# Kernel optimization log

Hardware: AMD Instinct MI355X
Metric: run time of the kernel (lower is better)

Reference implementation:

```python
import jax, jax.numpy as jnp
import numpy as np

B, T = 32768, 32
OBJ_V, PRED_V = 179, 46
E_OBJ, E_PRED, H = 5, 5, 32
IN_DIM = E_OBJ + E_PRED + 2 + 4  # 16, matches LSTMCell input size


def setup_inputs() -> dict:
    key = jax.random.key(0)
    ks = jax.random.split(key, 12)
    s = 0.1
    return {
        "input_objects": jax.random.randint(ks[0], (B, T), 0, OBJ_V),
        "input_boxes": jax.random.uniform(ks[1], (B, T, 4), dtype=jnp.float32),
        "predicates": jax.random.randint(ks[2], (B, T), 0, PRED_V),
        "subject_indicators": jax.random.randint(ks[3], (B, T), 0, 2),
        "target_object": jax.random.randint(ks[4], (B,), 0, OBJ_V),
        "obj_emb": jax.random.normal(ks[5], (OBJ_V, E_OBJ), dtype=jnp.float32) * s,
        "pred_emb": jax.random.normal(ks[6], (PRED_V, E_PRED), dtype=jnp.float32) * s,
        "W_ih": jax.random.normal(ks[7], (4 * H, IN_DIM), dtype=jnp.float32) * s,
        "W_hh": jax.random.normal(ks[8], (4 * H, H), dtype=jnp.float32) * s,
        "b_ih": jnp.zeros((4 * H,), dtype=jnp.float32),
        "b_hh": jnp.zeros((4 * H,), dtype=jnp.float32),
        "fc2_W": jax.random.normal(ks[9], (4, H), dtype=jnp.float32) * s,
        "fc2_b": jnp.zeros((4,), dtype=jnp.float32),
    }


def _forward(input_objects, input_boxes, predicates, subject_indicators,
             obj_emb, pred_emb, W_ih, W_hh, b_ih, b_hh, fc2_W, fc2_b):
    # concatenate_features, vectorized over all timesteps at once: [B,T,16]
    feats = jnp.concatenate([
        obj_emb[input_objects],                                   # [B,T,5]
        pred_emb[predicates],                                     # [B,T,5]
        jax.nn.one_hot(subject_indicators, 2, dtype=jnp.float32), # [B,T,2]
        input_boxes,                                              # [B,T,4]
    ], axis=-1)
    xs = jnp.transpose(feats, (1, 0, 2))  # [T,B,16] for scan over time

    def step(carry, x):
        h, c = carry
        gates = x @ W_ih.T + b_ih + h @ W_hh.T + b_hh  # [B,4H]
        i, f, g, o = jnp.split(gates, 4, axis=-1)      # torch gate order i,f,g,o
        i = jax.nn.sigmoid(i)
        f = jax.nn.sigmoid(f)
        g = jnp.tanh(g)
        o = jax.nn.sigmoid(o)
        c = f * c + i * g
        h = o * jnp.tanh(c)
        return (h, c), None

    h0 = jnp.zeros((input_objects.shape[0], H), dtype=jnp.float32)
    (h, _), _ = jax.lax.scan(step, (h0, h0), xs)
    out = h @ fc2_W.T + fc2_b          # output_fc2 on last hidden state
    return jnp.clip(out, 0.0, 1.0)     # torch.clamp(min=0, max=1)


def reference(input_objects, input_boxes, predicates, subject_indicators, target_object,
              obj_emb, pred_emb, W_ih, W_hh, b_ih, b_hh, fc2_W, fc2_b):
    # target_object is accepted by the torch forward but unused in its body
    return _forward(input_objects, input_boxes, predicates, subject_indicators,
                    obj_emb, pred_emb, W_ih, W_hh, b_ih, b_hh, fc2_W, fc2_b)
```

## Files before the change

### kernel.cpp

```cpp
#include <hip/hip_runtime.h>

#define XSTRIDE 1072
#define ZOFF    (16 * XSTRIDE)
#define LDS_BYTES (ZOFF + 32)

typedef _Float16 f16x8 __attribute__((ext_vector_type(8)));
typedef __fp16   fp16x2 __attribute__((ext_vector_type(2)));
typedef float    f32x4 __attribute__((ext_vector_type(4)));
typedef float    f32x2 __attribute__((ext_vector_type(2)));

#define LOG2E     1.44269504088896f
#define TWO_LOG2E 2.88539008177793f

__global__ __launch_bounds__(64, 2)
void lstm_fused(const int* __restrict__ objs,
                const float* __restrict__ boxes,
                const int* __restrict__ preds,
                const int* __restrict__ subj,
                const float* __restrict__ obj_emb,
                const float* __restrict__ pred_emb,
                const float* __restrict__ W_ih,
                const float* __restrict__ W_hh,
                const float* __restrict__ b_ih,
                const float* __restrict__ b_hh,
                const float* __restrict__ fc2_W,
                const float* __restrict__ fc2_b,
                float* __restrict__ out)
{
    extern __shared__ char smem[];
    const int lane = threadIdx.x;
    const int quad = lane >> 4;
    const int cidx = lane & 15;

    if (lane < 8) ((int*)(smem + ZOFF))[lane] = 0;

    {
        const int b = lane >> 2;
        const int j = lane & 3;
        const long gb = (long)blockIdx.x * 16 + b;
        const int* orow = objs + gb * 32;
        const int* prow = preds + gb * 32;
        const int* srow = subj + gb * 32;
        const float* brow = boxes + gb * 128;
        char* xrow = smem + b * XSTRIDE;
        #pragma unroll
        for (int tt = 0; tt < 8; ++tt) {
            int t = j + tt * 4;
            int o = orow[t], p = prow[t], sv = srow[t];
            const float* eo = obj_emb + o * 5;
            const float* ep = pred_emb + p * 5;
            float4 bx = *(const float4*)(brow + t * 4);
            f16x8 lo, hi;
            lo[0]=(_Float16)eo[0]; lo[1]=(_Float16)eo[1]; lo[2]=(_Float16)eo[2];
            lo[3]=(_Float16)eo[3]; lo[4]=(_Float16)eo[4];
            lo[5]=(_Float16)ep[0]; lo[6]=(_Float16)ep[1]; lo[7]=(_Float16)ep[2];
            hi[0]=(_Float16)ep[3]; hi[1]=(_Float16)ep[4];
            hi[2]=(_Float16)(sv==0 ? 1.0f : 0.0f);
            hi[3]=(_Float16)(sv==1 ? 1.0f : 0.0f);
            hi[4]=(_Float16)bx.x; hi[5]=(_Float16)bx.y;
            hi[6]=(_Float16)bx.z; hi[7]=(_Float16)bx.w;
            *(f16x8*)(xrow + t * 32)      = lo;
            *(f16x8*)(xrow + t * 32 + 16) = hi;
        }
    }

    f16x8 WH[8], WX[8];
    f32x4 bias[8];
    #pragma unroll
    for (int a = 0; a < 8; ++a) {
        const int gate = a >> 1;
        const float scale = (gate == 2) ? TWO_LOG2E : -LOG2E;
        const int n = gate * 32 + 8 * (cidx >> 2) + 4 * (a & 1) + (cidx & 3);
        const float* wr = W_hh + n * 32 + quad * 8;
        float4 w0 = *(const float4*)(wr);
        float4 w1 = *(const float4*)(wr + 4);
        f16x8 h8;
        h8[0]=(_Float16)(w0.x*scale); h8[1]=(_Float16)(w0.y*scale);
        h8[2]=(_Float16)(w0.z*scale); h8[3]=(_Float16)(w0.w*scale);
        h8[4]=(_Float16)(w1.x*scale); h8[5]=(_Float16)(w1.y*scale);
        h8[6]=(_Float16)(w1.z*scale); h8[7]=(_Float16)(w1.w*scale);
        WH[a] = h8;
        f16x8 x8;
        if (quad < 2) {
            const float* xr = W_ih + n * 16 + quad * 8;
            float4 u0 = *(const float4*)(xr);
            float4 u1 = *(const float4*)(xr + 4);
            x8[0]=(_Float16)(u0.x*scale); x8[1]=(_Float16)(u0.y*scale);
            x8[2]=(_Float16)(u0.z*scale); x8[3]=(_Float16)(u0.w*scale);
            x8[4]=(_Float16)(u1.x*scale); x8[5]=(_Float16)(u1.y*scale);
            x8[6]=(_Float16)(u1.z*scale); x8[7]=(_Float16)(u1.w*scale);
        } else {
            #pragma unroll
            for (int jj = 0; jj < 8; ++jj) x8[jj] = (_Float16)0.0f;
        }
        WX[a] = x8;
        const int nb = gate * 32 + 8 * quad + 4 * (a & 1);
        float4 bi = *(const float4*)(b_ih + nb);
        float4 bh = *(const float4*)(b_hh + nb);
        f32x4 bb = {(bi.x+bh.x)*scale, (bi.y+bh.y)*scale,
                    (bi.z+bh.z)*scale, (bi.w+bh.w)*scale};
        bias[a] = bb;
    }

    __syncthreads();

    const bool qlow = (quad < 2);
    int xaddr = qlow ? (cidx * XSTRIDE + quad * 16) : ZOFF;
    const int xinc = qlow ? 32 : 0;

    f16x8 xfrag = *(const f16x8*)(smem + xaddr); xaddr += xinc;
    f32x4 accp[8];
    #pragma unroll
    for (int a = 0; a < 8; ++a)
        accp[a] = __builtin_amdgcn_mfma_f32_16x16x32_f16(WX[a], xfrag, bias[a], 0, 0, 0);

    union { int i[4]; f16x8 v; } hf;
    hf.i[0]=0; hf.i[1]=0; hf.i[2]=0; hf.i[3]=0;
    const f32x2 zz = {0.0f, 0.0f};
    f32x2 cst[4] = {zz, zz, zz, zz};
    f32x2 hv[4];
    const f32x2 one = {1.0f, 1.0f};

    #pragma unroll 1
    for (int t = 0; t < 32; ++t) {
        f32x4 acc[8];
        #pragma unroll
        for (int a = 0; a < 8; ++a)
            acc[a] = __builtin_amdgcn_mfma_f32_16x16x32_f16(WH[a], hf.v, accp[a], 0, 0, 0);

        f16x8 xn = *(const f16x8*)(smem + xaddr); xaddr += xinc;

        #pragma unroll
        for (int cc = 0; cc < 4; ++cc) {
            const int sel = cc >> 1;
            const int r0  = (cc & 1) << 1;
            f32x2 zi = {acc[0+sel][r0], acc[0+sel][r0+1]};
            f32x2 zf = {acc[2+sel][r0], acc[2+sel][r0+1]};
            f32x2 zg = {acc[4+sel][r0], acc[4+sel][r0+1]};
            f32x2 zo = {acc[6+sel][r0], acc[6+sel][r0+1]};
            f32x2 Ei = {__builtin_amdgcn_exp2f(zi.x), __builtin_amdgcn_exp2f(zi.y)};
            f32x2 Ef = {__builtin_amdgcn_exp2f(zf.x), __builtin_amdgcn_exp2f(zf.y)};
            f32x2 Eg = {__builtin_amdgcn_exp2f(zg.x), __builtin_amdgcn_exp2f(zg.y)};
            f32x2 Eo = {__builtin_amdgcn_exp2f(zo.x), __builtin_amdgcn_exp2f(zo.y)};
            f32x2 t1  = Ei + one;
            f32x2 dig = t1 * Eg + t1;
            f32x2 tf  = Ef + one;
            f32x2 nn  = (Eg - one) * tf + cst[cc] * dig;
            f32x2 den = tf * dig;
            f32x2 rde = {__builtin_amdgcn_rcpf(den.x), __builtin_amdgcn_rcpf(den.y)};
            f32x2 c   = nn * rde;
            cst[cc] = c;
            f32x2 cl  = c * TWO_LOG2E;
            f32x2 Ec  = {__builtin_amdgcn_exp2f(cl.x), __builtin_amdgcn_exp2f(cl.y)};
            f32x2 to  = Eo + one;
            f32x2 dh  = to * Ec + to;
            f32x2 rdh = {__builtin_amdgcn_rcpf(dh.x), __builtin_amdgcn_rcpf(dh.y)};
            hv[cc] = (Ec - one) * rdh;
            union { fp16x2 h; int i; } pk;
            pk.h = __builtin_amdgcn_cvt_pkrtz(hv[cc].x, hv[cc].y);
            hf.i[cc] = pk.i;
        }

        #pragma unroll
        for (int a = 0; a < 8; ++a)
            accp[a] = __builtin_amdgcn_mfma_f32_16x16x32_f16(WX[a], xn, bias[a], 0, 0, 0);
    }

    __syncthreads();
    {
        char* s0 = smem + cidx * 144 + quad * 32;
        float4 lo4 = {hv[0].x, hv[0].y, hv[1].x, hv[1].y};
        float4 hi4 = {hv[2].x, hv[2].y, hv[3].x, hv[3].y};
        *(float4*)s0        = lo4;
        *(float4*)(s0 + 16) = hi4;
    }
    __syncthreads();
    {
        const int b = lane >> 2, j = lane & 3;
        const float* hrow = (const float*)(smem + b * 144);
        const float* fw = fc2_W + j * 32;
        float s = fc2_b[j];
        #pragma unroll
        for (int k = 0; k < 8; ++k) {
            float4 hvv = *(const float4*)(hrow + k * 4);
            float4 wv4 = *(const float4*)(fw + k * 4);
            s += wv4.x*hvv.x + wv4.y*hvv.y + wv4.z*hvv.z + wv4.w*hvv.w;
        }
        s = fminf(fmaxf(s, 0.0f), 1.0f);
        out[(long)blockIdx.x * 64 + lane] = s;
    }
}

extern "C" void kernel_launch(void* const* d_in, const int* in_sizes, int n_in,
                              void* d_out, int out_size, void* d_ws, size_t ws_size,
                              hipStream_t stream)
{
    lstm_fused<<<2048, 64, LDS_BYTES, stream>>>(
        (const int*)d_in[0], (const float*)d_in[1], (const int*)d_in[2],
        (const int*)d_in[3],
        (const float*)d_in[5], (const float*)d_in[6],
        (const float*)d_in[7], (const float*)d_in[8],
        (const float*)d_in[9], (const float*)d_in[10],
        (const float*)d_in[11], (const float*)d_in[12],
        (float*)d_out);
}
```

Baseline: 129.5 us.

## Switch LSTM recurrence to 32x32x16 MFMA with 32 batch rows per wave

Each wave now processes 32 batch rows instead of 16, using 32x32x16 f16 MFMA. The recurrent matmul splits into two chained MFMAs per gate over hidden halves, and the input projection needs no zero-padded fragment. Gate rows are permuted so each lane's accumulator rows line up with the next step's B-operand layout. The final FC is done in registers with a cross-half shuffle instead of an LDS round trip. The grid is halved and launch bounds drop to one wave per EU, which cuts parallelism across CUs and lengthens the serial chain per wave.

Result: slower. 135.7 us (+4.8%).

```diff
diff --git a/kernel.cpp b/kernel.cpp
--- a/kernel.cpp
+++ b/kernel.cpp
@@ -1,18 +1,27 @@
 #include <hip/hip_runtime.h>
 
-#define XSTRIDE 1072
-#define ZOFF    (16 * XSTRIDE)
-#define LDS_BYTES (ZOFF + 32)
+#define XSTRIDE 1040
+#define LDS_BYTES (32 * XSTRIDE)
 
 typedef _Float16 f16x8 __attribute__((ext_vector_type(8)));
 typedef __fp16   fp16x2 __attribute__((ext_vector_type(2)));
-typedef float    f32x4 __attribute__((ext_vector_type(4)));
+typedef float    f32x16 __attribute__((ext_vector_type(16)));
 typedef float    f32x2 __attribute__((ext_vector_type(2)));
 
 #define LOG2E     1.44269504088896f
 #define TWO_LOG2E 2.88539008177793f
 
-__global__ __launch_bounds__(64, 2)
+static __device__ __forceinline__ f16x8 cvt8(float4 a, float4 b, float s)
+{
+    f16x8 r;
+    r[0]=(_Float16)(a.x*s); r[1]=(_Float16)(a.y*s);
+    r[2]=(_Float16)(a.z*s); r[3]=(_Float16)(a.w*s);
+    r[4]=(_Float16)(b.x*s); r[5]=(_Float16)(b.y*s);
+    r[6]=(_Float16)(b.z*s); r[7]=(_Float16)(b.w*s);
+    return r;
+}
+
+__global__ __launch_bounds__(64, 1)
 void lstm_fused(const int* __restrict__ objs,
                 const float* __restrict__ boxes,
                 const int* __restrict__ preds,
@@ -29,115 +38,100 @@
 {
     extern __shared__ char smem[];
     const int lane = threadIdx.x;
-    const int quad = lane >> 4;
-    const int cidx = lane & 15;
-
-    if (lane < 8) ((int*)(smem + ZOFF))[lane] = 0;
+    const int hi   = lane >> 5;
+    const int col  = lane & 31;
 
     {
-        const int b = lane >> 2;
-        const int j = lane & 3;
-        const long gb = (long)blockIdx.x * 16 + b;
+        const int b = lane >> 1;
+        const int j = lane & 1;
+        const long gb = (long)blockIdx.x * 32 + b;
         const int* orow = objs + gb * 32;
         const int* prow = preds + gb * 32;
         const int* srow = subj + gb * 32;
         const float* brow = boxes + gb * 128;
         char* xrow = smem + b * XSTRIDE;
         #pragma unroll
-        for (int tt = 0; tt < 8; ++tt) {
-            int t = j + tt * 4;
+        for (int tt = 0; tt < 16; ++tt) {
+            int t = j + tt * 2;
             int o = orow[t], p = prow[t], sv = srow[t];
             const float* eo = obj_emb + o * 5;
             const float* ep = pred_emb + p * 5;
             float4 bx = *(const float4*)(brow + t * 4);
-            f16x8 lo, hi;
-            lo[0]=(_Float16)eo[0]; lo[1]=(_Float16)eo[1]; lo[2]=(_Float16)eo[2];
-            lo[3]=(_Float16)eo[3]; lo[4]=(_Float16)eo[4];
-            lo[5]=(_Float16)ep[0]; lo[6]=(_Float16)ep[1]; lo[7]=(_Float16)ep[2];
-            hi[0]=(_Float16)ep[3]; hi[1]=(_Float16)ep[4];
-            hi[2]=(_Float16)(sv==0 ? 1.0f : 0.0f);
-            hi[3]=(_Float16)(sv==1 ? 1.0f : 0.0f);
-            hi[4]=(_Float16)bx.x; hi[5]=(_Float16)bx.y;
-            hi[6]=(_Float16)bx.z; hi[7]=(_Float16)bx.w;
-            *(f16x8*)(xrow + t * 32)      = lo;
-            *(f16x8*)(xrow + t * 32 + 16) = hi;
-        }
-    }
-
-    f16x8 WH[8], WX[8];
-    f32x4 bias[8];
-    #pragma unroll
-    for (int a = 0; a < 8; ++a) {
-        const int gate = a >> 1;
-        const float scale = (gate == 2) ? TWO_LOG2E : -LOG2E;
-        const int n = gate * 32 + 8 * (cidx >> 2) + 4 * (a & 1) + (cidx & 3);
-        const float* wr = W_hh + n * 32 + quad * 8;
-        float4 w0 = *(const float4*)(wr);
-        float4 w1 = *(const float4*)(wr + 4);
-        f16x8 h8;
-        h8[0]=(_Float16)(w0.x*scale); h8[1]=(_Float16)(w0.y*scale);
-        h8[2]=(_Float16)(w0.z*scale); h8[3]=(_Float16)(w0.w*scale);
-        h8[4]=(_Float16)(w1.x*scale); h8[5]=(_Float16)(w1.y*scale);
-        h8[6]=(_Float16)(w1.z*scale); h8[7]=(_Float16)(w1.w*scale);
-        WH[a] = h8;
-        f16x8 x8;
-        if (quad < 2) {
-            const float* xr = W_ih + n * 16 + quad * 8;
-            float4 u0 = *(const float4*)(xr);
-            float4 u1 = *(const float4*)(xr + 4);
-            x8[0]=(_Float16)(u0.x*scale); x8[1]=(_Float16)(u0.y*scale);
-            x8[2]=(_Float16)(u0.z*scale); x8[3]=(_Float16)(u0.w*scale);
-            x8[4]=(_Float16)(u1.x*scale); x8[5]=(_Float16)(u1.y*scale);
-            x8[6]=(_Float16)(u1.z*scale); x8[7]=(_Float16)(u1.w*scale);
-        } else {
-            #pragma unroll
-            for (int jj = 0; jj < 8; ++jj) x8[jj] = (_Float16)0.0f;
-        }
-        WX[a] = x8;
-        const int nb = gate * 32 + 8 * quad + 4 * (a & 1);
-        float4 bi = *(const float4*)(b_ih + nb);
-        float4 bh = *(const float4*)(b_hh + nb);
-        f32x4 bb = {(bi.x+bh.x)*scale, (bi.y+bh.y)*scale,
-                    (bi.z+bh.z)*scale, (bi.w+bh.w)*scale};
-        bias[a] = bb;
+            f16x8 lo8, hi8;
+            lo8[0]=(_Float16)eo[0]; lo8[1]=(_Float16)eo[1]; lo8[2]=(_Float16)eo[2];
+            lo8[3]=(_Float16)eo[3]; lo8[4]=(_Float16)eo[4];
+            lo8[5]=(_Float16)ep[0]; lo8[6]=(_Float16)ep[1]; lo8[7]=(_Float16)ep[2];
+            hi8[0]=(_Float16)ep[3]; hi8[1]=(_Float16)ep[4];
+            hi8[2]=(_Float16)(sv==0 ? 1.0f : 0.0f);
+            hi8[3]=(_Float16)(sv==1 ? 1.0f : 0.0f);
+            hi8[4]=(_Float16)bx.x; hi8[5]=(_Float16)bx.y;
+            hi8[6]=(_Float16)bx.z; hi8[7]=(_Float16)bx.w;
+            *(f16x8*)(xrow + t * 32)      = lo8;
+            *(f16x8*)(xrow + t * 32 + 16) = hi8;
+        }
+    }
+
+    const int bb = col >> 2;
+    const int bp = (bb & 4) | ((bb & 1) << 1) | ((bb >> 1) & 1);
+    const int up = (col & 3) | (bp << 2);
+    f16x8 WH0[4], WH1[4], WX[4];
+    f32x16 bias[4];
+    #pragma unroll
+    for (int a = 0; a < 4; ++a) {
+        const float scale = (a == 2) ? TWO_LOG2E : -LOG2E;
+        const int n = a * 32 + up;
+        const float* wh = W_hh + n * 32 + 8 * hi;
+        WH0[a] = cvt8(*(const float4*)(wh),      *(const float4*)(wh + 4),  scale);
+        WH1[a] = cvt8(*(const float4*)(wh + 16), *(const float4*)(wh + 20), scale);
+        const float* wx = W_ih + n * 16 + 8 * hi;
+        WX[a]  = cvt8(*(const float4*)(wx),      *(const float4*)(wx + 4),  scale);
+        const float* bi = b_ih + a * 32;
+        const float* bh = b_hh + a * 32;
+        #pragma unroll
+        for (int r = 0; r < 8; ++r)
+            bias[a][r]     = (bi[8*hi + r]      + bh[8*hi + r])      * scale;
+        #pragma unroll
+        for (int r = 0; r < 8; ++r)
+            bias[a][8 + r] = (bi[16 + 8*hi + r] + bh[16 + 8*hi + r]) * scale;
     }
 
     __syncthreads();
 
-    const bool qlow = (quad < 2);
-    int xaddr = qlow ? (cidx * XSTRIDE + quad * 16) : ZOFF;
-    const int xinc = qlow ? 32 : 0;
-
-    f16x8 xfrag = *(const f16x8*)(smem + xaddr); xaddr += xinc;
-    f32x4 accp[8];
-    #pragma unroll
-    for (int a = 0; a < 8; ++a)
-        accp[a] = __builtin_amdgcn_mfma_f32_16x16x32_f16(WX[a], xfrag, bias[a], 0, 0, 0);
-
-    union { int i[4]; f16x8 v; } hf;
-    hf.i[0]=0; hf.i[1]=0; hf.i[2]=0; hf.i[3]=0;
+    int xaddr = col * XSTRIDE + hi * 16;
+    f16x8 xfrag = *(const f16x8*)(smem + xaddr); xaddr += 32;
+    f32x16 accp[4];
+    #pragma unroll
+    for (int a = 0; a < 4; ++a)
+        accp[a] = __builtin_amdgcn_mfma_f32_32x32x16_f16(WX[a], xfrag, bias[a], 0, 0, 0);
+
+    union u32x4 { int i[4]; f16x8 v; };
+    u32x4 hB0, hB1;
+    hB0.i[0]=0; hB0.i[1]=0; hB0.i[2]=0; hB0.i[3]=0;
+    hB1.i[0]=0; hB1.i[1]=0; hB1.i[2]=0; hB1.i[3]=0;
     const f32x2 zz = {0.0f, 0.0f};
-    f32x2 cst[4] = {zz, zz, zz, zz};
-    f32x2 hv[4];
+    f32x2 cst[8] = {zz, zz, zz, zz, zz, zz, zz, zz};
+    f32x2 hv[8];
     const f32x2 one = {1.0f, 1.0f};
 
     #pragma unroll 1
     for (int t = 0; t < 32; ++t) {
-        f32x4 acc[8];
-        #pragma unroll
-        for (int a = 0; a < 8; ++a)
-            acc[a] = __builtin_amdgcn_mfma_f32_16x16x32_f16(WH[a], hf.v, accp[a], 0, 0, 0);
-
-        f16x8 xn = *(const f16x8*)(smem + xaddr); xaddr += xinc;
-
-        #pragma unroll
-        for (int cc = 0; cc < 4; ++cc) {
-            const int sel = cc >> 1;
-            const int r0  = (cc & 1) << 1;
-            f32x2 zi = {acc[0+sel][r0], acc[0+sel][r0+1]};
-            f32x2 zf = {acc[2+sel][r0], acc[2+sel][r0+1]};
-            f32x2 zg = {acc[4+sel][r0], acc[4+sel][r0+1]};
-            f32x2 zo = {acc[6+sel][r0], acc[6+sel][r0+1]};
+        f32x16 acc[4];
+        #pragma unroll
+        for (int a = 0; a < 4; ++a) {
+            f32x16 tmp = __builtin_amdgcn_mfma_f32_32x32x16_f16(WH0[a], hB0.v, accp[a], 0, 0, 0);
+            acc[a]     = __builtin_amdgcn_mfma_f32_32x32x16_f16(WH1[a], hB1.v, tmp,     0, 0, 0);
+        }
+
+        f16x8 xn = *(const f16x8*)(smem + xaddr); xaddr += 32;
+
+        u32x4 nb0, nb1;
+        #pragma unroll
+        for (int r = 0; r < 8; ++r) {
+            const int r0 = 2 * r;
+            f32x2 zi = {acc[0][r0], acc[0][r0+1]};
+            f32x2 zf = {acc[1][r0], acc[1][r0+1]};
+            f32x2 zg = {acc[2][r0], acc[2][r0+1]};
+            f32x2 zo = {acc[3][r0], acc[3][r0+1]};
             f32x2 Ei = {__builtin_amdgcn_exp2f(zi.x), __builtin_amdgcn_exp2f(zi.y)};
             f32x2 Ef = {__builtin_amdgcn_exp2f(zf.x), __builtin_amdgcn_exp2f(zf.y)};
             f32x2 Eg = {__builtin_amdgcn_exp2f(zg.x), __builtin_amdgcn_exp2f(zg.y)};
@@ -145,49 +139,55 @@
             f32x2 t1  = Ei + one;
             f32x2 dig = t1 * Eg + t1;
             f32x2 tf  = Ef + one;
-            f32x2 nn  = (Eg - one) * tf + cst[cc] * dig;
+            f32x2 nn  = (Eg - one) * tf + cst[r] * dig;
             f32x2 den = tf * dig;
             f32x2 rde = {__builtin_amdgcn_rcpf(den.x), __builtin_amdgcn_rcpf(den.y)};
             f32x2 c   = nn * rde;
-            cst[cc] = c;
+            cst[r] = c;
             f32x2 cl  = c * TWO_LOG2E;
             f32x2 Ec  = {__builtin_amdgcn_exp2f(cl.x), __builtin_amdgcn_exp2f(cl.y)};
             f32x2 to  = Eo + one;
             f32x2 dh  = to * Ec + to;
             f32x2 rdh = {__builtin_amdgcn_rcpf(dh.x), __builtin_amdgcn_rcpf(dh.y)};
-            hv[cc] = (Ec - one) * rdh;
+            hv[r] = (Ec - one) * rdh;
             union { fp16x2 h; int i; } pk;
-            pk.h = __builtin_amdgcn_cvt_pkrtz(hv[cc].x, hv[cc].y);
-            hf.i[cc] = pk.i;
-        }
-
-        #pragma unroll
-        for (int a = 0; a < 8; ++a)
-            accp[a] = __builtin_amdgcn_mfma_f32_16x16x32_f16(WX[a], xn, bias[a], 0, 0, 0);
-    }
-
-    __syncthreads();
-    {
-        char* s0 = smem + cidx * 144 + quad * 32;
-        float4 lo4 = {hv[0].x, hv[0].y, hv[1].x, hv[1].y};
-        float4 hi4 = {hv[2].x, hv[2].y, hv[3].x, hv[3].y};
-        *(float4*)s0        = lo4;
-        *(float4*)(s0 + 16) = hi4;
-    }
-    __syncthreads();
-    {
-        const int b = lane >> 2, j = lane & 3;
-        const float* hrow = (const float*)(smem + b * 144);
+            pk.h = __builtin_amdgcn_cvt_pkrtz(hv[r].x, hv[r].y);
+            if (r < 4) nb0.i[r] = pk.i; else nb1.i[r - 4] = pk.i;
+        }
+        hB0 = nb0; hB1 = nb1;
+
+        #pragma unroll
+        for (int a = 0; a < 4; ++a)
+            accp[a] = __builtin_amdgcn_mfma_f32_32x32x16_f16(WX[a], xn, bias[a], 0, 0, 0);
+    }
+
+    float p[4];
+    #pragma unroll
+    for (int j = 0; j < 4; ++j) {
         const float* fw = fc2_W + j * 32;
-        float s = fc2_b[j];
-        #pragma unroll
-        for (int k = 0; k < 8; ++k) {
-            float4 hvv = *(const float4*)(hrow + k * 4);
-            float4 wv4 = *(const float4*)(fw + k * 4);
-            s += wv4.x*hvv.x + wv4.y*hvv.y + wv4.z*hvv.z + wv4.w*hvv.w;
-        }
-        s = fminf(fmaxf(s, 0.0f), 1.0f);
-        out[(long)blockIdx.x * 64 + lane] = s;
+        float s = 0.0f;
+        #pragma unroll
+        for (int r = 0; r < 4; ++r) {
+            s += fw[8*hi + 2*r]     * hv[r].x;
+            s += fw[8*hi + 2*r + 1] * hv[r].y;
+        }
+        #pragma unroll
+        for (int r = 4; r < 8; ++r) {
+            s += fw[16 + 8*hi + 2*(r-4)]     * hv[r].x;
+            s += fw[16 + 8*hi + 2*(r-4) + 1] * hv[r].y;
+        }
+        p[j] = s;
+    }
+    #pragma unroll
+    for (int j = 0; j < 4; ++j)
+        p[j] += __shfl_xor(p[j], 32);
+    if (lane < 32) {
+        float4 o4;
+        o4.x = fminf(fmaxf(p[0] + fc2_b[0], 0.0f), 1.0f);
+        o4.y = fminf(fmaxf(p[1] + fc2_b[1], 0.0f), 1.0f);
+        o4.z = fminf(fmaxf(p[2] + fc2_b[2], 0.0f), 1.0f);
+        o4.w = fminf(fmaxf(p[3] + fc2_b[3], 0.0f), 1.0f);
+        *(float4*)(out + ((long)blockIdx.x * 32 + col) * 4) = o4;
     }
 }
 
@@ -195,7 +195,7 @@
                               void* d_out, int out_size, void* d_ws, size_t ws_size,
                               hipStream_t stream)
 {
-    lstm_fused<<<2048, 64, LDS_BYTES, stream>>>(
+    lstm_fused<<<1024, 64, LDS_BYTES, stream>>>(
         (const int*)d_in[0], (const float*)d_in[1], (const int*)d_in[2],
         (const int*)d_in[3],
         (const float*)d_in[5], (const float*)d_in[6],
```

## Split feature gather into a separate pack kernel writing fp16 rows to workspace

Applied to the files above, without the earlier changes.

Moves the embedding gather, one-hot and box packing out of the LSTM kernel into a separate high-occupancy pack_x kernel. That kernel writes fp16 feature rows to the workspace, and the LSTM kernel then copies them into LDS with coalesced 16-byte loads. The aim is to take the latency-bound scattered gathers out of the low-occupancy 64-thread LSTM blocks. The cost is an extra launch and a round trip of 32 MB through global memory. If the workspace is too small, a monolithic fallback kernel is used instead.

Result: slower. 144.3 us (+11.4%).

```diff
diff --git a/kernel.cpp b/kernel.cpp
--- a/kernel.cpp
+++ b/kernel.cpp
@@ -12,13 +12,47 @@
 #define LOG2E     1.44269504088896f
 #define TWO_LOG2E 2.88539008177793f
 
+__global__ __launch_bounds__(256)
+void pack_x(const int* __restrict__ objs,
+            const float* __restrict__ boxes,
+            const int* __restrict__ preds,
+            const int* __restrict__ subj,
+            const float* __restrict__ obj_emb,
+            const float* __restrict__ pred_emb,
+            char* __restrict__ ws)
+{
+    const int gid = blockIdx.x * 256 + threadIdx.x;
+    const long b  = gid >> 4;
+    const int  t0 = (gid & 15) << 1;
+    int2 ov = *(const int2*)(objs  + b * 32 + t0);
+    int2 pv = *(const int2*)(preds + b * 32 + t0);
+    int2 sv = *(const int2*)(subj  + b * 32 + t0);
+    int oarr[2] = {ov.x, ov.y};
+    int parr[2] = {pv.x, pv.y};
+    int sarr[2] = {sv.x, sv.y};
+    #pragma unroll
+    for (int tt = 0; tt < 2; ++tt) {
+        int t = t0 + tt;
+        const float* eo = obj_emb  + oarr[tt] * 5;
+        const float* ep = pred_emb + parr[tt] * 5;
+        float4 bx = *(const float4*)(boxes + (b * 32 + t) * 4);
+        f16x8 lo, hi;
+        lo[0]=(_Float16)eo[0]; lo[1]=(_Float16)eo[1]; lo[2]=(_Float16)eo[2];
+        lo[3]=(_Float16)eo[3]; lo[4]=(_Float16)eo[4];
+        lo[5]=(_Float16)ep[0]; lo[6]=(_Float16)ep[1]; lo[7]=(_Float16)ep[2];
+        hi[0]=(_Float16)ep[3]; hi[1]=(_Float16)ep[4];
+        hi[2]=(_Float16)(sarr[tt]==0 ? 1.0f : 0.0f);
+        hi[3]=(_Float16)(sarr[tt]==1 ? 1.0f : 0.0f);
+        hi[4]=(_Float16)bx.x; hi[5]=(_Float16)bx.y;
+        hi[6]=(_Float16)bx.z; hi[7]=(_Float16)bx.w;
+        char* dst = ws + b * 1024 + t * 32;
+        *(f16x8*)dst        = lo;
+        *(f16x8*)(dst + 16) = hi;
+    }
+}
+
 __global__ __launch_bounds__(64, 2)
-void lstm_fused(const int* __restrict__ objs,
-                const float* __restrict__ boxes,
-                const int* __restrict__ preds,
-                const int* __restrict__ subj,
-                const float* __restrict__ obj_emb,
-                const float* __restrict__ pred_emb,
+void lstm_fused(const char* __restrict__ ws,
                 const float* __restrict__ W_ih,
                 const float* __restrict__ W_hh,
                 const float* __restrict__ b_ih,
@@ -35,32 +69,14 @@
     if (lane < 8) ((int*)(smem + ZOFF))[lane] = 0;
 
     {
-        const int b = lane >> 2;
-        const int j = lane & 3;
-        const long gb = (long)blockIdx.x * 16 + b;
-        const int* orow = objs + gb * 32;
-        const int* prow = preds + gb * 32;
-        const int* srow = subj + gb * 32;
-        const float* brow = boxes + gb * 128;
-        char* xrow = smem + b * XSTRIDE;
-        #pragma unroll
-        for (int tt = 0; tt < 8; ++tt) {
-            int t = j + tt * 4;
-            int o = orow[t], p = prow[t], sv = srow[t];
-            const float* eo = obj_emb + o * 5;
-            const float* ep = pred_emb + p * 5;
-            float4 bx = *(const float4*)(brow + t * 4);
-            f16x8 lo, hi;
-            lo[0]=(_Float16)eo[0]; lo[1]=(_Float16)eo[1]; lo[2]=(_Float16)eo[2];
-            lo[3]=(_Float16)eo[3]; lo[4]=(_Float16)eo[4];
-            lo[5]=(_Float16)ep[0]; lo[6]=(_Float16)ep[1]; lo[7]=(_Float16)ep[2];
-            hi[0]=(_Float16)ep[3]; hi[1]=(_Float16)ep[4];
-            hi[2]=(_Float16)(sv==0 ? 1.0f : 0.0f);
-            hi[3]=(_Float16)(sv==1 ? 1.0f : 0.0f);
-            hi[4]=(_Float16)bx.x; hi[5]=(_Float16)bx.y;
-            hi[6]=(_Float16)bx.z; hi[7]=(_Float16)bx.w;
-            *(f16x8*)(xrow + t * 32)      = lo;
-            *(f16x8*)(xrow + t * 32 + 16) = hi;
+        const char* wsrc = ws + (long)blockIdx.x * 16 * 1024;
+        #pragma unroll
+        for (int it = 0; it < 16; ++it) {
+            int c   = lane + (it << 6);
+            int row = c >> 6;
+            int off = (c & 63) << 4;
+            *(f16x8*)(smem + row * XSTRIDE + off) =
+                *(const f16x8*)(wsrc + ((long)c << 4));
         }
     }
 
@@ -191,16 +207,199 @@
     }
 }
 
+__global__ __launch_bounds__(64, 2)
+void lstm_mono(const int* __restrict__ objs,
+               const float* __restrict__ boxes,
+               const int* __restrict__ preds,
+               const int* __restrict__ subj,
+               const float* __restrict__ obj_emb,
+               const float* __restrict__ pred_emb,
+               const float* __restrict__ W_ih,
+               const float* __restrict__ W_hh,
+               const float* __restrict__ b_ih,
+               const float* __restrict__ b_hh,
+               const float* __restrict__ fc2_W,
+               const float* __restrict__ fc2_b,
+               float* __restrict__ out)
+{
+    extern __shared__ char smem[];
+    const int lane = threadIdx.x;
+    const int quad = lane >> 4;
+    const int cidx = lane & 15;
+
+    if (lane < 8) ((int*)(smem + ZOFF))[lane] = 0;
+    {
+        const int b = lane >> 2;
+        const int j = lane & 3;
+        const long gb = (long)blockIdx.x * 16 + b;
+        const int* orow = objs + gb * 32;
+        const int* prow = preds + gb * 32;
+        const int* srow = subj + gb * 32;
+        const float* brow = boxes + gb * 128;
+        char* xrow = smem + b * XSTRIDE;
+        #pragma unroll
+        for (int tt = 0; tt < 8; ++tt) {
+            int t = j + tt * 4;
+            int o = orow[t], p = prow[t], sv = srow[t];
+            const float* eo = obj_emb + o * 5;
+            const float* ep = pred_emb + p * 5;
+            float4 bx = *(const float4*)(brow + t * 4);
+            f16x8 lo, hi;
+            lo[0]=(_Float16)eo[0]; lo[1]=(_Float16)eo[1]; lo[2]=(_Float16)eo[2];
+            lo[3]=(_Float16)eo[3]; lo[4]=(_Float16)eo[4];
+            lo[5]=(_Float16)ep[0]; lo[6]=(_Float16)ep[1]; lo[7]=(_Float16)ep[2];
+            hi[0]=(_Float16)ep[3]; hi[1]=(_Float16)ep[4];
+            hi[2]=(_Float16)(sv==0 ? 1.0f : 0.0f);
+            hi[3]=(_Float16)(sv==1 ? 1.0f : 0.0f);
+            hi[4]=(_Float16)bx.x; hi[5]=(_Float16)bx.y;
+            hi[6]=(_Float16)bx.z; hi[7]=(_Float16)bx.w;
+            *(f16x8*)(xrow + t * 32)      = lo;
+            *(f16x8*)(xrow + t * 32 + 16) = hi;
+        }
+    }
+    f16x8 WH[8], WX[8];
+    f32x4 bias[8];
+    #pragma unroll
+    for (int a = 0; a < 8; ++a) {
+        const int gate = a >> 1;
+        const float scale = (gate == 2) ? TWO_LOG2E : -LOG2E;
+        const int n = gate * 32 + 8 * (cidx >> 2) + 4 * (a & 1) + (cidx & 3);
+        const float* wr = W_hh + n * 32 + quad * 8;
+        float4 w0 = *(const float4*)(wr);
+        float4 w1 = *(const float4*)(wr + 4);
+        f16x8 h8;
+        h8[0]=(_Float16)(w0.x*scale); h8[1]=(_Float16)(w0.y*scale);
+        h8[2]=(_Float16)(w0.z*scale); h8[3]=(_Float16)(w0.w*scale);
+        h8[4]=(_Float16)(w1.x*scale); h8[5]=(_Float16)(w1.y*scale);
+        h8[6]=(_Float16)(w1.z*scale); h8[7]=(_Float16)(w1.w*scale);
+        WH[a] = h8;
+        f16x8 x8;
+        if (quad < 2) {
+            const float* xr = W_ih + n * 16 + quad * 8;
+            float4 u0 = *(const float4*)(xr);
+            float4 u1 = *(const float4*)(xr + 4);
+            x8[0]=(_Float16)(u0.x*scale); x8[1]=(_Float16)(u0.y*scale);
+            x8[2]=(_Float16)(u0.z*scale); x8[3]=(_Float16)(u0.w*scale);
+            x8[4]=(_Float16)(u1.x*scale); x8[5]=(_Float16)(u1.y*scale);
+            x8[6]=(_Float16)(u1.z*scale); x8[7]=(_Float16)(u1.w*scale);
+        } else {
+            #pragma unroll
+            for (int jj = 0; jj < 8; ++jj) x8[jj] = (_Float16)0.0f;
+        }
+        WX[a] = x8;
+        const int nb = gate * 32 + 8 * quad + 4 * (a & 1);
+        float4 bi = *(const float4*)(b_ih + nb);
+        float4 bh = *(const float4*)(b_hh + nb);
+        f32x4 bb = {(bi.x+bh.x)*scale, (bi.y+bh.y)*scale,
+                    (bi.z+bh.z)*scale, (bi.w+bh.w)*scale};
+        bias[a] = bb;
+    }
+    __syncthreads();
+    const bool qlow = (quad < 2);
+    int xaddr = qlow ? (cidx * XSTRIDE + quad * 16) : ZOFF;
+    const int xinc = qlow ? 32 : 0;
+    f16x8 xfrag = *(const f16x8*)(smem + xaddr); xaddr += xinc;
+    f32x4 accp[8];
+    #pragma unroll
+    for (int a = 0; a < 8; ++a)
+        accp[a] = __builtin_amdgcn_mfma_f32_16x16x32_f16(WX[a], xfrag, bias[a], 0, 0, 0);
+    union { int i[4]; f16x8 v; } hf;
+    hf.i[0]=0; hf.i[1]=0; hf.i[2]=0; hf.i[3]=0;
+    const f32x2 zz = {0.0f, 0.0f};
+    f32x2 cst[4] = {zz, zz, zz, zz};
+    f32x2 hv[4];
+    const f32x2 one = {1.0f, 1.0f};
+    #pragma unroll 1
+    for (int t = 0; t < 32; ++t) {
+        f32x4 acc[8];
+        #pragma unroll
+        for (int a = 0; a < 8; ++a)
+            acc[a] = __builtin_amdgcn_mfma_f32_16x16x32_f16(WH[a], hf.v, accp[a], 0, 0, 0);
+        f16x8 xn = *(const f16x8*)(smem + xaddr); xaddr += xinc;
+        #pragma unroll
+        for (int cc = 0; cc < 4; ++cc) {
+            const int sel = cc >> 1;
+            const int r0  = (cc & 1) << 1;
+            f32x2 zi = {acc[0+sel][r0], acc[0+sel][r0+1]};
+            f32x2 zf = {acc[2+sel][r0], acc[2+sel][r0+1]};
+            f32x2 zg = {acc[4+sel][r0], acc[4+sel][r0+1]};
+            f32x2 zo = {acc[6+sel][r0], acc[6+sel][r0+1]};
+            f32x2 Ei = {__builtin_amdgcn_exp2f(zi.x), __builtin_amdgcn_exp2f(zi.y)};
+            f32x2 Ef = {__builtin_amdgcn_exp2f(zf.x), __builtin_amdgcn_exp2f(zf.y)};
+            f32x2 Eg = {__builtin_amdgcn_exp2f(zg.x), __builtin_amdgcn_exp2f(zg.y)};
+            f32x2 Eo = {__builtin_amdgcn_exp2f(zo.x), __builtin_amdgcn_exp2f(zo.y)};
+            f32x2 t1  = Ei + one;
+            f32x2 dig = t1 * Eg + t1;
+            f32x2 tf  = Ef + one;
+            f32x2 nn  = (Eg - one) * tf + cst[cc] * dig;
+            f32x2 den = tf * dig;
+            f32x2 rde = {__builtin_amdgcn_rcpf(den.x), __builtin_amdgcn_rcpf(den.y)};
+            f32x2 c   = nn * rde;
+            cst[cc] = c;
+            f32x2 cl  = c * TWO_LOG2E;
+            f32x2 Ec  = {__builtin_amdgcn_exp2f(cl.x), __builtin_amdgcn_exp2f(cl.y)};
+            f32x2 to  = Eo + one;
+            f32x2 dh  = to * Ec + to;
+            f32x2 rdh = {__builtin_amdgcn_rcpf(dh.x), __builtin_amdgcn_rcpf(dh.y)};
+            hv[cc] = (Ec - one) * rdh;
+            union { fp16x2 h; int i; } pk;
+            pk.h = __builtin_amdgcn_cvt_pkrtz(hv[cc].x, hv[cc].y);
+            hf.i[cc] = pk.i;
+        }
+        #pragma unroll
+        for (int a = 0; a < 8; ++a)
+            accp[a] = __builtin_amdgcn_mfma_f32_16x16x32_f16(WX[a], xn, bias[a], 0, 0, 0);
+    }
+    __syncthreads();
+    {
+        char* s0 = smem + cidx * 144 + quad * 32;
+        float4 lo4 = {hv[0].x, hv[0].y, hv[1].x, hv[1].y};
+        float4 hi4 = {hv[2].x, hv[2].y, hv[3].x, hv[3].y};
+        *(float4*)s0        = lo4;
+        *(float4*)(s0 + 16) = hi4;
+    }
+    __syncthreads();
+    {
+        const int b = lane >> 2, j = lane & 3;
+        const float* hrow = (const float*)(smem + b * 144);
+        const float* fw = fc2_W + j * 32;
+        float s = fc2_b[j];
+        #pragma unroll
+        for (int k = 0; k < 8; ++k) {
+            float4 hvv = *(const float4*)(hrow + k * 4);
+            float4 wv4 = *(const float4*)(fw + k * 4);
+            s += wv4.x*hvv.x + wv4.y*hvv.y + wv4.z*hvv.z + wv4.w*hvv.w;
+        }
+        s = fminf(fmaxf(s, 0.0f), 1.0f);
+        out[(long)blockIdx.x * 64 + lane] = s;
+    }
+}
+
 extern "C" void kernel_launch(void* const* d_in, const int* in_sizes, int n_in,
                               void* d_out, int out_size, void* d_ws, size_t ws_size,
                               hipStream_t stream)
 {
-    lstm_fused<<<2048, 64, LDS_BYTES, stream>>>(
-        (const int*)d_in[0], (const float*)d_in[1], (const int*)d_in[2],
-        (const int*)d_in[3],
-        (const float*)d_in[5], (const float*)d_in[6],
-        (const float*)d_in[7], (const float*)d_in[8],
-        (const float*)d_in[9], (const float*)d_in[10],
-        (const float*)d_in[11], (const float*)d_in[12],
-        (float*)d_out);
+    const size_t WS_NEEDED = (size_t)32768 * 1024;
+    if (ws_size >= WS_NEEDED && d_ws != nullptr) {
+        pack_x<<<2048, 256, 0, stream>>>(
+            (const int*)d_in[0], (const float*)d_in[1], (const int*)d_in[2],
+            (const int*)d_in[3],
+            (const float*)d_in[5], (const float*)d_in[6],
+            (char*)d_ws);
+        lstm_fused<<<2048, 64, LDS_BYTES, stream>>>(
+            (const char*)d_ws,
+            (const float*)d_in[7], (const float*)d_in[8],
+            (const float*)d_in[9], (const float*)d_in[10],
+            (const float*)d_in[11], (const float*)d_in[12],
+            (float*)d_out);
+    } else {
+        lstm_mono<<<2048, 64, LDS_BYTES, stream>>>(
+            (const int*)d_in[0], (const float*)d_in[1], (const int*)d_in[2],
+            (const int*)d_in[3],
+            (const float*)d_in[5], (const float*)d_in[6],
+            (const float*)d_in[7], (const float*)d_in[8],
+            (const float*)d_in[9], (const float*)d_in[10],
+            (const float*)d_in[11], (const float*)d_in[12],
+            (float*)d_out);
+    }
 }
```
